# Performance work log

Hardware: AMD Instinct MI355X
Metric: run time of the kernel (lower is better)

Reference implementation:

```python
import jax, jax.numpy as jnp
import numpy as np

B, S, HIDDEN, N_HEADS = 1, 2048, 2048, 16
HEAD_DIM = HIDDEN // N_HEADS  # 128


def setup_inputs() -> dict:
    key = jax.random.key(0)
    ks = jax.random.split(key, 7)
    w = 0.02  # init scale for projection weights
    return {
        "x_self": jax.random.normal(ks[0], (B, S, HIDDEN), jnp.float32),
        "x_cross": jax.random.normal(ks[1], (B, S, HIDDEN), jnp.float32),
        "mask": jnp.zeros((B, 1, S, S), jnp.float32),
        "Wq": jax.random.normal(ks[2], (HIDDEN, HIDDEN), jnp.float32) * w,
        "Wk": jax.random.normal(ks[3], (HIDDEN, HIDDEN), jnp.float32) * w,
        "Wv": jax.random.normal(ks[4], (HIDDEN, HIDDEN), jnp.float32) * w,
        "Wo": jax.random.normal(ks[5], (HIDDEN, HIDDEN), jnp.float32) * w,
    }


def reference(x_self, x_cross, mask, Wq, Wk, Wv, Wo):
    bf16 = jnp.bfloat16
    b = x_self.shape[0]
    scale = HEAD_DIM ** -0.5

    def split_heads(x):  # [b, s, hidden] -> [b, h, s, d]
        return x.reshape(b, -1, N_HEADS, HEAD_DIM).transpose(0, 2, 1, 3)

    # projections run in bf16 (weights cast to bf16 in the original)
    q_self = split_heads((x_self.astype(bf16) @ Wq.astype(bf16).T))
    q_cross = split_heads((x_cross.astype(bf16) @ Wq.astype(bf16).T))
    # k/v for both self and cross blocks come from x_self with identical weights
    k = split_heads((x_self.astype(bf16) @ Wk.astype(bf16).T))
    v = split_heads((x_self.astype(bf16) @ Wv.astype(bf16).T))

    def attn_block(qh):
        # fp32 upcast for QK^T + softmax, then bf16 cast for AV (dropout p=0 -> identity)
        w = jnp.einsum('bhqd,bhkd->bhqk', qh.astype(jnp.float32), k.astype(jnp.float32)) * scale
        w = w + mask
        w = jax.nn.softmax(w, axis=-1).astype(bf16)
        return jnp.einsum('bhqk,bhkd->bhqd', w, v.astype(bf16))  # [b, h, s, d] bf16

    out_self = attn_block(q_self)
    out_cross = attn_block(q_cross)
    out = jnp.concatenate([out_self, out_cross], axis=1)          # [b, 2h, s, d]
    out_flat = out.transpose(0, 2, 1, 3).reshape(b, -1, HIDDEN)   # [b, 2s, hidden]
    Wo_bf = Wo.astype(bf16)
    out_final = 0.5 * (out_flat @ Wo_bf.T + out_flat @ Wo_bf.T)
    return out_final.astype(jnp.float32)
```

## Files before the change

### kernel.cpp

```cpp
#include <hip/hip_runtime.h>
#include <hip/hip_bf16.h>
#include <stdint.h>

#define S 2048
#define HID 2048
#define NH 16
#define HD 128

typedef short short8 __attribute__((ext_vector_type(8)));
typedef float f32x4 __attribute__((ext_vector_type(4)));
typedef float f32x16 __attribute__((ext_vector_type(16)));
typedef uint32_t u32;
typedef u32 u32x4 __attribute__((ext_vector_type(4)));

__device__ __forceinline__ ushort f2bf(float x) {
  uint32_t u = __builtin_bit_cast(uint32_t, x);
  if ((u & 0x7fffffffu) > 0x7f800000u) return (ushort)((u >> 16) | 0x40);
  uint32_t r = u + 0x7fffu + ((u >> 16) & 1u);
  return (ushort)(r >> 16);
}
__device__ __forceinline__ float bf2f(ushort u) {
  union { uint32_t i; float f; } c; c.i = ((uint32_t)u) << 16; return c.f;
}

__device__ __forceinline__ void glds16(const ushort* g, ushort* l) {
  __builtin_amdgcn_global_load_lds((const __attribute__((address_space(1))) uint32_t*)g,
                                   (__attribute__((address_space(3))) uint32_t*)l, 16, 0, 0);
}

__device__ __forceinline__ void mfma16(f32x4& d, short8 a, short8 b) {
  asm("v_mfma_f32_16x16x32_bf16 %0, %1, %2, %0" : "+v"(d) : "v"(a), "v"(b));
}
__device__ __forceinline__ void mfma32(f32x16& d, short8 a, short8 b) {
  asm("v_mfma_f32_32x32x16_bf16 %0, %1, %2, %0" : "+v"(d) : "v"(a), "v"(b));
}
__device__ __forceinline__ void plswap(u32& a, u32& b) {
  asm("v_permlane32_swap_b32 %0, %1" : "+v"(a), "+v"(b));
}
__device__ __forceinline__ u32 cvtpk(float lo, float hi) {
  u32 r; asm("v_cvt_pk_bf16_f32 %0, %1, %2" : "=v"(r) : "v"(lo), "v"(hi)); return r;
}

struct CastArgs { const float* s[6]; ushort* d[6]; };
__global__ __launch_bounds__(256) void cast6_k(CastArgs a) {
  const float* in = a.s[blockIdx.y];
  ushort* out = a.d[blockIdx.y];
  int i = blockIdx.x * 256 + threadIdx.x;
  float4 v = ((const float4*)in)[i];
  ushort4 o;
  o.x = f2bf(v.x); o.y = f2bf(v.y); o.z = f2bf(v.z); o.w = f2bf(v.w);
  ((ushort4*)out)[i] = o;
}

template <int OUTF32, int NSPLIT>
__global__ __launch_bounds__(256)
void gemm_bt_k(const ushort* __restrict__ A, const ushort* __restrict__ B,
               void* __restrict__ C, int M, int N, int K) {
  __shared__ __align__(16) ushort ldsA[128 * 64];
  __shared__ __align__(16) ushort ldsB[128 * 64];
  const int tid = threadIdx.x, lane = tid & 63, wid = tid >> 6;
  const int g = lane >> 4, c = lane & 15;
  const int wr = wid >> 1, wc = wid & 1;
  const long m0 = (long)blockIdx.y * 128, n0 = (long)blockIdx.x * 128;
  const int srow = lane >> 3, sslot = lane & 7;

  f32x4 acc[4][4] = {};

  for (int k0 = 0; k0 < K; k0 += 64) {
#pragma unroll
    for (int i = 0; i < 4; ++i) {
      int ii = wid * 4 + i;
      int rt = ii * 8 + srow;
      int col = ((sslot ^ (rt & 7)) << 3) + k0;
      glds16(A + (m0 + rt) * (long)K + col, ldsA + ii * 512);
      glds16(B + (n0 + rt) * (long)K + col, ldsB + ii * 512);
    }
    __syncthreads();
#pragma unroll
    for (int kk = 0; kk < 2; ++kk) {
      short8 af[4], bfr[4];
#pragma unroll
      for (int m = 0; m < 4; ++m) {
        int row = wr * 64 + m * 16 + c;
        af[m] = *(const short8*)(ldsA + row * 64 + (((kk * 4 + g) ^ (row & 7)) << 3));
      }
#pragma unroll
      for (int n = 0; n < 4; ++n) {
        int row = wc * 64 + n * 16 + c;
        bfr[n] = *(const short8*)(ldsB + row * 64 + (((kk * 4 + g) ^ (row & 7)) << 3));
      }
#pragma unroll
      for (int m = 0; m < 4; ++m)
#pragma unroll
        for (int n = 0; n < 4; ++n) mfma16(acc[m][n], af[m], bfr[n]);
    }
    __syncthreads();
  }
  asm volatile("s_nop 7\n\ts_nop 7");
#pragma unroll
  for (int m = 0; m < 4; ++m) {
#pragma unroll
    for (int r = 0; r < 4; ++r) {
      long grow = m0 + wr * 64 + m * 16 + g * 4 + r;
#pragma unroll
      for (int n = 0; n < 4; ++n) {
        long gcol = n0 + wc * 64 + n * 16 + c;
        long idx;
        if (NSPLIT) idx = ((gcol >> 11) << 22) + (grow << 11) + (gcol & 2047);
        else        idx = grow * N + gcol;
        float v = acc[m][n][r];
        if (OUTF32) ((float*)C)[idx] = bf2f(f2bf(v));
        else        ((ushort*)C)[idx] = f2bf(v);
      }
    }
  }
}

__global__ __launch_bounds__(256)
void transpose_bf16_k(const ushort* __restrict__ in, ushort* __restrict__ out) {
  __shared__ __align__(16) ushort t[64][72];
  const int tid = threadIdx.x;
  const long bx = (long)blockIdx.x * 64;
  const long by = (long)blockIdx.y * 64;
#pragma unroll
  for (int i = 0; i < 2; ++i) {
    int row = (tid >> 3) + i * 32;
    int col = (tid & 7) * 8;
    *(short8*)(&t[row][col]) = *(const short8*)(in + (by + row) * 2048 + bx + col);
  }
  __syncthreads();
#pragma unroll
  for (int i = 0; i < 2; ++i) {
    int orow = (tid >> 3) + i * 32;
    int ocol = (tid & 7) * 8;
    short8 v;
#pragma unroll
    for (int j = 0; j < 8; ++j) v[j] = (short)t[ocol + j][orow];
    *(short8*)(out + (bx + orow) * 2048 + by + ocol) = v;
  }
}

__global__ __launch_bounds__(512)
void attn3_k(const ushort* __restrict__ Qself, const ushort* __restrict__ Qcross,
             const ushort* __restrict__ Kp, const ushort* __restrict__ Vt,
             const float* __restrict__ mask, ushort* __restrict__ outf) {
  __shared__ __align__(16) ushort ldsK[2 * 64 * 128];
  __shared__ __align__(16) ushort ldsV[2 * 128 * 64];
  const int tid = threadIdx.x, lane = tid & 63, wid = tid >> 6;
  const int c31 = lane & 31, hi = lane >> 5;
  const int h = blockIdx.y, blk = blockIdx.z;
  const ushort* Qp = blk ? Qcross : Qself;
  const int qbase = blockIdx.x * 256 + wid * 32;
  const long qme = qbase + c31;

  short8 qf[8];
#pragma unroll
  for (int ks = 0; ks < 8; ++ks)
    qf[ks] = *(const short8*)(Qp + qme * HID + h * HD + ks * 16 + hi * 8);

  f32x16 o[4] = {};
  float m_r = -__builtin_inff(), l_r = 0.f;

  const float SC  = 0.08838834764831845f;
  const float L2E = 1.4426950408889634f;
  const float THR = 5.545177444479562f;

  const int kRow4 = lane >> 4, kSlot = lane & 15;
  const int vRow8 = lane >> 3, vSlot = lane & 7;
  const float* mrow = mask + qme * (long)S;

#define STAGE(BO, KV0) do {                                                       \
    _Pragma("unroll")                                                             \
    for (int i_ = 0; i_ < 2; ++i_) {                                              \
      int seg = i_ * 8 + wid;                                                     \
      int rk = seg * 4 + kRow4;                                                   \
      glds16(Kp + (long)((KV0) + rk) * HID + h * HD + ((kSlot ^ (rk & 15)) << 3), \
             ldsK + (BO) * 8192 + seg * 512);                                     \
      int rv = seg * 8 + vRow8;                                                   \
      glds16(Vt + (long)(h * HD + rv) * S + (KV0) + ((vSlot ^ (rv & 7)) << 3),    \
             ldsV + (BO) * 8192 + seg * 512);                                     \
    }                                                                             \
  } while (0)

  STAGE(0, 0);
  __syncthreads();

  for (int t = 0; t < 32; ++t) {
    const int bo = t & 1;
    const ushort* kb = ldsK + bo * 8192;
    const ushort* vb = ldsV + bo * 8192;
    if (t < 31) STAGE(bo ^ 1, (t + 1) * 64);
    const int kv0 = t * 64;

    f32x4 mv[2][4];
#pragma unroll
    for (int kvb = 0; kvb < 2; ++kvb)
#pragma unroll
      for (int rg = 0; rg < 4; ++rg)
        mv[kvb][rg] = *(const f32x4*)(mrow + kv0 + kvb * 32 + rg * 8 + hi * 4);

    f32x16 s0 = {}, s1 = {};
    __builtin_amdgcn_s_setprio(1);
#pragma unroll
    for (int ks = 0; ks < 8; ++ks) {
      int r0 = c31, r1 = 32 + c31;
      short8 kf0 = *(const short8*)(kb + r0 * 128 + (((ks * 2 + hi) ^ (r0 & 15)) << 3));
      short8 kf1 = *(const short8*)(kb + r1 * 128 + (((ks * 2 + hi) ^ (r1 & 15)) << 3));
      mfma32(s0, kf0, qf[ks]);
      mfma32(s1, kf1, qf[ks]);
    }
    __builtin_amdgcn_s_setprio(0);
    asm volatile("s_nop 7\n\ts_nop 7");

#pragma unroll
    for (int r = 0; r < 16; ++r) {
      s0[r] = __builtin_fmaf(s0[r], SC, mv[0][r >> 2][r & 3]);
      s1[r] = __builtin_fmaf(s1[r], SC, mv[1][r >> 2][r & 3]);
    }

    float pmax = s0[0];
#pragma unroll
    for (int r = 1; r < 16; ++r) pmax = fmaxf(pmax, s0[r]);
#pragma unroll
    for (int r = 0; r < 16; ++r) pmax = fmaxf(pmax, s1[r]);
    pmax = fmaxf(pmax, __shfl_xor(pmax, 32));

    if (!__all(pmax <= m_r + THR)) {
      float mnew = fmaxf(m_r, pmax);
      float alpha = __builtin_amdgcn_exp2f((m_r - mnew) * L2E);
      m_r = mnew;
      l_r *= alpha;
#pragma unroll
      for (int r = 0; r < 16; ++r) {
        float alf = __shfl(alpha, (r & 3) + 8 * (r >> 2) + 4 * hi);
#pragma unroll
        for (int dt = 0; dt < 4; ++dt) o[dt][r] *= alf;
      }
    }

    const float nm = -m_r * L2E;
    float lsum = 0.f;
#pragma unroll
    for (int r = 0; r < 16; ++r) {
      s0[r] = __builtin_amdgcn_exp2f(__builtin_fmaf(s0[r], L2E, nm)); lsum += s0[r];
      s1[r] = __builtin_amdgcn_exp2f(__builtin_fmaf(s1[r], L2E, nm)); lsum += s1[r];
    }
    lsum += __shfl_xor(lsum, 32);
    l_r += lsum;

    short8 pa[4];
#pragma unroll
    for (int kk = 0; kk < 4; ++kk) {
      const f32x16& sv = (kk < 2) ? s0 : s1;
      const int b = (kk & 1) * 8;
      u32 x0 = cvtpk(sv[b + 0], sv[b + 1]);
      u32 x1 = cvtpk(sv[b + 2], sv[b + 3]);
      u32 y0 = cvtpk(sv[b + 4], sv[b + 5]);
      u32 y1 = cvtpk(sv[b + 6], sv[b + 7]);
      plswap(x0, y0);
      plswap(x1, y1);
      u32x4 tt; tt[0] = x0; tt[1] = x1; tt[2] = y0; tt[3] = y1;
      pa[kk] = __builtin_bit_cast(short8, tt);
    }
    asm volatile("s_nop 3");

    __builtin_amdgcn_s_setprio(1);
#pragma unroll
    for (int dt = 0; dt < 4; ++dt) {
      int row = dt * 32 + c31;
#pragma unroll
      for (int kk = 0; kk < 4; ++kk) {
        short8 vf = *(const short8*)(vb + row * 64 + (((kk * 2 + hi) ^ (row & 7)) << 3));
        mfma32(o[dt], pa[kk], vf);
      }
    }
    __builtin_amdgcn_s_setprio(0);

    __syncthreads();
  }
#undef STAGE

  asm volatile("s_nop 7\n\ts_nop 7");
#pragma unroll
  for (int r = 0; r < 16; ++r) {
    int qr = (r & 3) + 8 * (r >> 2) + 4 * hi;
    float linv = 1.0f / __shfl(l_r, qr);
    long orow = 2L * (qbase + qr) + blk;
#pragma unroll
    for (int dt = 0; dt < 4; ++dt)
      outf[orow * HID + h * HD + dt * 32 + c31] = f2bf(o[dt][r] * linv);
  }
}

extern "C" void kernel_launch(void* const* d_in, const int* in_sizes, int n_in,
                              void* d_out, int out_size, void* d_ws, size_t ws_size,
                              hipStream_t stream) {
  (void)in_sizes; (void)n_in; (void)out_size; (void)ws_size;
  const float* x_self  = (const float*)d_in[0];
  const float* x_cross = (const float*)d_in[1];
  const float* mask    = (const float*)d_in[2];
  const float* Wq      = (const float*)d_in[3];
  const float* Wk      = (const float*)d_in[4];
  const float* Wv      = (const float*)d_in[5];
  const float* Wo      = (const float*)d_in[6];

  uint8_t* w = (uint8_t*)d_ws;
  const size_t MB8 = (size_t)S * HID * sizeof(ushort);
  ushort* xs_bf   = (ushort*)(w + 0 * MB8);
  ushort* xc_bf   = (ushort*)(w + 1 * MB8);
  ushort* Wq_bf   = (ushort*)(w + 2 * MB8);
  ushort* Wk_bf   = (ushort*)(w + 3 * MB8);
  ushort* Wv_bf   = (ushort*)(w + 4 * MB8);
  ushort* Wo_bf   = (ushort*)(w + 5 * MB8);
  ushort* q_self  = (ushort*)(w + 6 * MB8);
  ushort* q_cross = (ushort*)(w + 7 * MB8);
  ushort* k_      = (ushort*)(w + 8 * MB8);
  ushort* v_      = (ushort*)(w + 9 * MB8);
  ushort* vt       = xs_bf;
  ushort* out_flat = Wq_bf;

  CastArgs ca;
  ca.s[0] = x_self;  ca.d[0] = xs_bf;
  ca.s[1] = x_cross; ca.d[1] = xc_bf;
  ca.s[2] = Wq;      ca.d[2] = Wq_bf;
  ca.s[3] = Wk;      ca.d[3] = Wk_bf;
  ca.s[4] = Wv;      ca.d[4] = Wv_bf;
  ca.s[5] = Wo;      ca.d[5] = Wo_bf;
  cast6_k<<<dim3(4096, 6), 256, 0, stream>>>(ca);

  gemm_bt_k<0, 0><<<dim3(16, 32), 256, 0, stream>>>(xs_bf, Wq_bf, q_self, 4096, 2048, 2048);
  gemm_bt_k<0, 1><<<dim3(32, 16), 256, 0, stream>>>(xs_bf, Wk_bf, k_, 2048, 4096, 2048);

  transpose_bf16_k<<<dim3(32, 32), 256, 0, stream>>>(v_, vt);

  attn3_k<<<dim3(8, 16, 2), 512, 0, stream>>>(q_self, q_cross, k_, vt, mask, out_flat);

  gemm_bt_k<1, 0><<<dim3(16, 32), 256, 0, stream>>>(out_flat, Wo_bf, d_out, 4096, 2048, 2048);
}
```

Measured before the change: 265.5 us.

## Shrink attention blocks to 4 waves and remap grid for XCD-local heads

The attention kernel now runs 256-thread blocks that each cover 128 query rows, and launches 512 blocks on a flat grid. Block indices are decoded so that consecutive blocks on the same XCD share a head, which should improve L2 reuse of that head's K/V tiles and give more, smaller blocks. The row max and row sum are now computed with tree reductions instead of serial chains to shorten dependency latency. Inline asm is made volatile and sched_barrier fences are added around MFMA hazards, trading scheduling freedom for predictable ordering. Each block now issues more staging loads per thread and K/V is loaded redundantly by twice as many blocks.

```diff
diff --git a/kernel.cpp b/kernel.cpp
--- a/kernel.cpp
+++ b/kernel.cpp
@@ -29,16 +29,20 @@
 }
 
 __device__ __forceinline__ void mfma16(f32x4& d, short8 a, short8 b) {
-  asm("v_mfma_f32_16x16x32_bf16 %0, %1, %2, %0" : "+v"(d) : "v"(a), "v"(b));
+  asm volatile("v_mfma_f32_16x16x32_bf16 %0, %1, %2, %0" : "+v"(d) : "v"(a), "v"(b));
 }
 __device__ __forceinline__ void mfma32(f32x16& d, short8 a, short8 b) {
-  asm("v_mfma_f32_32x32x16_bf16 %0, %1, %2, %0" : "+v"(d) : "v"(a), "v"(b));
-}
+  asm volatile("v_mfma_f32_32x32x16_bf16 %0, %1, %2, %0" : "+v"(d) : "v"(a), "v"(b));
+}
+#define MFMA_FENCE() do {                              \
+    asm volatile("s_nop 7\n\ts_nop 7\n\ts_nop 7");     \
+    __builtin_amdgcn_sched_barrier(0);                 \
+  } while (0)
 __device__ __forceinline__ void plswap(u32& a, u32& b) {
-  asm("v_permlane32_swap_b32 %0, %1" : "+v"(a), "+v"(b));
+  asm volatile("v_permlane32_swap_b32 %0, %1" : "+v"(a), "+v"(b));
 }
 __device__ __forceinline__ u32 cvtpk(float lo, float hi) {
-  u32 r; asm("v_cvt_pk_bf16_f32 %0, %1, %2" : "=v"(r) : "v"(lo), "v"(hi)); return r;
+  u32 r; asm volatile("v_cvt_pk_bf16_f32 %0, %1, %2" : "=v"(r) : "v"(lo), "v"(hi)); return r;
 }
 
 struct CastArgs { const float* s[6]; ushort* d[6]; };
@@ -96,7 +100,7 @@
     }
     __syncthreads();
   }
-  asm volatile("s_nop 7\n\ts_nop 7");
+  MFMA_FENCE();
 #pragma unroll
   for (int m = 0; m < 4; ++m) {
 #pragma unroll
@@ -140,17 +144,23 @@
   }
 }
 
-__global__ __launch_bounds__(512)
-void attn3_k(const ushort* __restrict__ Qself, const ushort* __restrict__ Qcross,
+__global__ __launch_bounds__(256)
+void attn4_k(const ushort* __restrict__ Qself, const ushort* __restrict__ Qcross,
              const ushort* __restrict__ Kp, const ushort* __restrict__ Vt,
              const float* __restrict__ mask, ushort* __restrict__ outf) {
   __shared__ __align__(16) ushort ldsK[2 * 64 * 128];
   __shared__ __align__(16) ushort ldsV[2 * 128 * 64];
   const int tid = threadIdx.x, lane = tid & 63, wid = tid >> 6;
   const int c31 = lane & 31, hi = lane >> 5;
-  const int h = blockIdx.y, blk = blockIdx.z;
+
+  const int b = blockIdx.x;
+  const int xcd = b & 7, j = b >> 3;
+  const int h = xcd + 8 * (j & 1);
+  const int blk = (j >> 1) & 1;
+  const int qt = j >> 2;
+
   const ushort* Qp = blk ? Qcross : Qself;
-  const int qbase = blockIdx.x * 256 + wid * 32;
+  const int qbase = qt * 128 + wid * 32;
   const long qme = qbase + c31;
 
   short8 qf[8];
@@ -171,8 +181,8 @@
 
 #define STAGE(BO, KV0) do {                                                       \
     _Pragma("unroll")                                                             \
-    for (int i_ = 0; i_ < 2; ++i_) {                                              \
-      int seg = i_ * 8 + wid;                                                     \
+    for (int i_ = 0; i_ < 4; ++i_) {                                              \
+      int seg = i_ * 4 + wid;                                                     \
       int rk = seg * 4 + kRow4;                                                   \
       glds16(Kp + (long)((KV0) + rk) * HID + h * HD + ((kSlot ^ (rk & 15)) << 3), \
              ldsK + (BO) * 8192 + seg * 512);                                     \
@@ -210,7 +220,7 @@
       mfma32(s1, kf1, qf[ks]);
     }
     __builtin_amdgcn_s_setprio(0);
-    asm volatile("s_nop 7\n\ts_nop 7");
+    MFMA_FENCE();
 
 #pragma unroll
     for (int r = 0; r < 16; ++r) {
@@ -218,12 +228,15 @@
       s1[r] = __builtin_fmaf(s1[r], SC, mv[1][r >> 2][r & 3]);
     }
 
-    float pmax = s0[0];
-#pragma unroll
-    for (int r = 1; r < 16; ++r) pmax = fmaxf(pmax, s0[r]);
-#pragma unroll
-    for (int r = 0; r < 16; ++r) pmax = fmaxf(pmax, s1[r]);
-    pmax = fmaxf(pmax, __shfl_xor(pmax, 32));
+    float mx[16];
+#pragma unroll
+    for (int r = 0; r < 16; ++r) mx[r] = fmaxf(s0[r], s1[r]);
+#pragma unroll
+    for (int st = 8; st >= 1; st >>= 1)
+#pragma unroll
+      for (int i = 0; i < 8; ++i)
+        if (i < st) mx[i] = fmaxf(mx[i], mx[i + st]);
+    float pmax = fmaxf(mx[0], __shfl_xor(mx[0], 32));
 
     if (!__all(pmax <= m_r + THR)) {
       float mnew = fmaxf(m_r, pmax);
@@ -239,30 +252,37 @@
     }
 
     const float nm = -m_r * L2E;
-    float lsum = 0.f;
 #pragma unroll
     for (int r = 0; r < 16; ++r) {
-      s0[r] = __builtin_amdgcn_exp2f(__builtin_fmaf(s0[r], L2E, nm)); lsum += s0[r];
-      s1[r] = __builtin_amdgcn_exp2f(__builtin_fmaf(s1[r], L2E, nm)); lsum += s1[r];
-    }
-    lsum += __shfl_xor(lsum, 32);
-    l_r += lsum;
+      s0[r] = __builtin_amdgcn_exp2f(__builtin_fmaf(s0[r], L2E, nm));
+      s1[r] = __builtin_amdgcn_exp2f(__builtin_fmaf(s1[r], L2E, nm));
+    }
+    float sm[16];
+#pragma unroll
+    for (int r = 0; r < 16; ++r) sm[r] = s0[r] + s1[r];
+#pragma unroll
+    for (int st = 8; st >= 1; st >>= 1)
+#pragma unroll
+      for (int i = 0; i < 8; ++i)
+        if (i < st) sm[i] += sm[i + st];
+    l_r += sm[0] + __shfl_xor(sm[0], 32);
 
     short8 pa[4];
 #pragma unroll
     for (int kk = 0; kk < 4; ++kk) {
       const f32x16& sv = (kk < 2) ? s0 : s1;
-      const int b = (kk & 1) * 8;
-      u32 x0 = cvtpk(sv[b + 0], sv[b + 1]);
-      u32 x1 = cvtpk(sv[b + 2], sv[b + 3]);
-      u32 y0 = cvtpk(sv[b + 4], sv[b + 5]);
-      u32 y1 = cvtpk(sv[b + 6], sv[b + 7]);
+      const int bq = (kk & 1) * 8;
+      u32 x0 = cvtpk(sv[bq + 0], sv[bq + 1]);
+      u32 x1 = cvtpk(sv[bq + 2], sv[bq + 3]);
+      u32 y0 = cvtpk(sv[bq + 4], sv[bq + 5]);
+      u32 y1 = cvtpk(sv[bq + 6], sv[bq + 7]);
       plswap(x0, y0);
       plswap(x1, y1);
       u32x4 tt; tt[0] = x0; tt[1] = x1; tt[2] = y0; tt[3] = y1;
       pa[kk] = __builtin_bit_cast(short8, tt);
     }
-    asm volatile("s_nop 3");
+    asm volatile("s_nop 1");
+    __builtin_amdgcn_sched_barrier(0);
 
     __builtin_amdgcn_s_setprio(1);
 #pragma unroll
@@ -280,7 +300,7 @@
   }
 #undef STAGE
 
-  asm volatile("s_nop 7\n\ts_nop 7");
+  MFMA_FENCE();
 #pragma unroll
   for (int r = 0; r < 16; ++r) {
     int qr = (r & 3) + 8 * (r >> 2) + 4 * hi;
@@ -333,7 +353,7 @@
 
   transpose_bf16_k<<<dim3(32, 32), 256, 0, stream>>>(v_, vt);
 
-  attn3_k<<<dim3(8, 16, 2), 512, 0, stream>>>(q_self, q_cross, k_, vt, mask, out_flat);
+  attn4_k<<<dim3(512), 256, 0, stream>>>(q_self, q_cross, k_, vt, mask, out_flat);
 
   gemm_bt_k<1, 0><<<dim3(16, 32), 256, 0, stream>>>(out_flat, Wo_bf, d_out, 4096, 2048, 2048);
 }
```

Measured after the change: 256.7 us. 1.03x faster.
